# Kernel tuning notes

Hardware: AMD Instinct MI355X
Metric: run time of the kernel (lower is better)

The kernel has to match this reference:

```python
import jax, jax.numpy as jnp
import numpy as np

TOL = 1e-3


def _image_grads(F):
    # replicate-pad central difference, matches GradientBatch (conv with [-0.5,0,0.5])
    Fx = jnp.pad(F, ((0, 0), (0, 0), (0, 0), (1, 1)), mode='edge')
    gx = 0.5 * (Fx[:, :, :, 2:] - Fx[:, :, :, :-2])
    Fy = jnp.pad(F, ((0, 0), (0, 0), (1, 1), (0, 0)), mode='edge')
    gy = 0.5 * (Fy[:, :, 2:, :] - Fy[:, :, :-2, :])
    return gx, gy


def _param_to_H(p):
    B = p.shape[0]
    z = jnp.zeros((B, 1, 1), p.dtype)
    return jnp.concatenate([p, z], 1).reshape(B, 3, 3) + jnp.eye(3, dtype=p.dtype)


def _bilinear_sample(A, xw, yw):
    # grid_sample(mode='bilinear', align_corners=True, padding_mode='zeros') at pixel coords (xw, yw)
    B, k, h, w = A.shape
    x0 = jnp.floor(xw)
    y0 = jnp.floor(yw)
    fx = (xw - x0).reshape(B, 1, h * w)
    fy = (yw - y0).reshape(B, 1, h * w)
    Af = A.reshape(B, k, h * w)

    def gather(xi, yi):
        valid = (xi >= 0) & (xi <= w - 1) & (yi >= 0) & (yi <= h - 1)
        xi_c = jnp.clip(xi, 0, w - 1).astype(jnp.int32)
        yi_c = jnp.clip(yi, 0, h - 1).astype(jnp.int32)
        idx = (yi_c * w + xi_c).reshape(B, 1, h * w)
        v = jnp.take_along_axis(Af, jnp.broadcast_to(idx, (B, k, h * w)), axis=2)
        return v * valid.reshape(B, 1, h * w).astype(A.dtype)

    v00 = gather(x0, y0)
    v01 = gather(x0 + 1, y0)
    v10 = gather(x0, y0 + 1)
    v11 = gather(x0 + 1, y0 + 1)
    Q = ((1 - fx) * (1 - fy) * v00 + fx * (1 - fy) * v01
         + (1 - fx) * fy * v10 + fx * fy * v11)
    return Q.reshape(B, k, h, w)


def _deeplk(img, temp, init_param, max_itr):
    B, k, h, w = temp.shape
    dt = temp.dtype
    gx, gy = _image_grads(temp)
    # centered pixel grid (meshgrid in source: x - x.max()/2)
    x = jnp.arange(w, dtype=dt) - (w - 1) / 2.0
    y = jnp.arange(h, dtype=dt) - (h - 1) / 2.0
    X, Y = jnp.meshgrid(x, y)  # (h, w); X varies along w
    Xf = jnp.tile(X.reshape(-1), k)  # [k*h*w], tiled per channel
    Yf = jnp.tile(Y.reshape(-1), k)
    gxf = gx.reshape(B, k * h * w)
    gyf = gy.reshape(B, k * h * w)
    dIdp = jnp.stack([
        Xf * gxf, Yf * gxf, gxf,
        Xf * gyf, Yf * gyf, gyf,
        -Xf * Xf * gxf - Xf * Yf * gyf,
        -Xf * Yf * gxf - Yf * Yf * gyf,
    ], axis=2)  # [B, k*h*w, 8]
    Hmat = jnp.einsum('bnp,bnq->bpq', dIdp, dIdp)  # [B,8,8]
    invH = jnp.linalg.inv(Hmat)
    invH_dIdp = jnp.einsum('bpq,bnq->bpn', invH, dIdp)  # [B,8,k*h*w]
    xy = jnp.stack([X.reshape(-1), Y.reshape(-1), jnp.ones((h * w,), dt)], 0)  # [3, h*w]
    tolf = jnp.asarray(TOL, dt)

    def step(carry, _):
        p, dp = carry
        Hm = _param_to_H(p)
        xyw = jnp.einsum('bij,jn->bin', Hm, xy)  # [B,3,h*w]
        Xw = (xyw[:, 0] / xyw[:, 2]).reshape(B, h, w) + (w - 1) / 2.0
        Yw = (xyw[:, 1] / xyw[:, 2]).reshape(B, h, w) + (h - 1) / 2.0
        Fi_warp = _bilinear_sample(img, Xw, Yw)
        xn = Xw / ((w - 1) / 2.0) - 1.0
        yn = Yw / ((h - 1) / 2.0) - 1.0
        mask = ((xn > -1 + 2.0 / w) & (xn < 1 - 2.0 / w)
                & (yn > -1 + 2.0 / h) & (yn < 1 - 2.0 / h)).astype(dt)
        r = (Fi_warp - temp * mask[:, None]).reshape(B, k * h * w, 1)
        dp_new = jnp.einsum('bpn,bnj->bpj', invH_dIdp, r)  # [B,8,1]
        dp_new = dp_new.at[:, 6:8, 0].set(0.0)  # zero projective terms
        active = (jnp.linalg.norm(dp, axis=1, keepdims=True) > tolf).astype(dt)
        dp2 = active * dp_new  # converged samples freeze (dp stays 0)
        return (p - dp2, dp2), None

    dp0 = jnp.ones((B, 8, 1), dt)
    (p, _), _ = jax.lax.scan(step, (init_param, dp0), None, length=max_itr)
    return p


def setup_inputs() -> dict:
    key = jax.random.key(0)
    k1, k2 = jax.random.split(key)
    B, k, h, w = 8, 8, 256, 256
    img = jax.random.normal(k1, (B, k, h, w), dtype=jnp.float32)
    temp = jax.random.normal(k2, (B, k, h, w), dtype=jnp.float32)
    init_param = jnp.zeros((B, 8, 1), dtype=jnp.float32)
    return {"img": img, "temp": temp, "init_param": init_param, "max_itr": 10}


def reference(img, temp, init_param, max_itr):
    p = _deeplk(img, temp, init_param, max_itr)
    return (p, _param_to_H(p))
```

## Files before the change

### kernel.cpp

```cpp
#include <hip/hip_runtime.h>
#include <hip/hip_bf16.h>

#define B_ 8
#define K_ 8
#define H_ 256
#define W_ 256
#define HW (H_*W_)

__device__ __forceinline__ unsigned short f2bf(float f) {
    __hip_bfloat16 h = __float2bfloat16(f);
    return *reinterpret_cast<unsigned short*>(&h);
}
__device__ __forceinline__ void ub8(uint4 u, float* o) {
    o[0] = __uint_as_float(u.x << 16); o[1] = __uint_as_float(u.x & 0xffff0000u);
    o[2] = __uint_as_float(u.y << 16); o[3] = __uint_as_float(u.y & 0xffff0000u);
    o[4] = __uint_as_float(u.z << 16); o[5] = __uint_as_float(u.z & 0xffff0000u);
    o[6] = __uint_as_float(u.w << 16); o[7] = __uint_as_float(u.w & 0xffff0000u);
}
__device__ __forceinline__ float half_reduce(float v) {
    v += __shfl_down(v, 16, 64);
    v += __shfl_down(v, 8, 64);
    v += __shfl_down(v, 4, 64);
    v += __shfl_down(v, 2, 64);
    v += __shfl_down(v, 1, 64);
    return v;
}
__device__ __forceinline__ void cstore(float* p, float v) {
    __hip_atomic_store(p, v, __ATOMIC_RELAXED, __HIP_MEMORY_SCOPE_AGENT);
}
__device__ __forceinline__ float cload(const float* p) {
    return __hip_atomic_load((float*)p, __ATOMIC_RELAXED, __HIP_MEMORY_SCOPE_AGENT);
}
__device__ __forceinline__ void wait_count(unsigned int* p, unsigned int target) {
    for (int i = 0; i < 1000000; ++i) {
        if (__hip_atomic_load(p, __ATOMIC_RELAXED, __HIP_MEMORY_SCOPE_AGENT) >= target)
            return;
        __builtin_amdgcn_s_sleep(1);
    }
}

__device__ __forceinline__ void pixel_accum(
    const uint4* __restrict__ imgT,
    const uint4 t0, const uint4 g0, const uint4 g1,
    int b, int x, int y,
    float h00, float h01, float h02, float h10, float h11, float h12,
    float h20, float h21, float* aa) {
    const float X = (float)x - 127.5f, Y = (float)y - 127.5f;
    const float zw = h20 * X + h21 * Y + 1.f;
    const float Xw = (h00 * X + h01 * Y + h02) / zw + 127.5f;
    const float Yw = (h10 * X + h11 * Y + h12) / zw + 127.5f;
    const float NLO = -1.f + 2.f / 256.f, NHI = 1.f - 2.f / 256.f;
    const float xn = Xw / 127.5f - 1.f, yn = Yw / 127.5f - 1.f;
    const float m = (xn > NLO && xn < NHI && yn > NLO && yn < NHI) ? 1.f : 0.f;

    const float x0f = floorf(Xw), y0f = floorf(Yw);
    const float fx = Xw - x0f, fy = Yw - y0f;
    const float x1f = x0f + 1.f, y1f = y0f + 1.f;
    const bool vx0 = (x0f >= 0.f) && (x0f <= 255.f);
    const bool vx1 = (x1f >= 0.f) && (x1f <= 255.f);
    const bool vy0 = (y0f >= 0.f) && (y0f <= 255.f);
    const bool vy1 = (y1f >= 0.f) && (y1f <= 255.f);
    const int xi0 = (int)fminf(fmaxf(x0f, 0.f), 255.f);
    const int xi1 = (int)fminf(fmaxf(x1f, 0.f), 255.f);
    const int yi0 = (int)fminf(fmaxf(y0f, 0.f), 255.f);
    const int yi1 = (int)fminf(fmaxf(y1f, 0.f), 255.f);
    const int i00 = yi0 * W_ + xi0, i01 = yi0 * W_ + xi1;
    const int i10 = yi1 * W_ + xi0, i11 = yi1 * W_ + xi1;
    const float w00 = ((vx0 && vy0) ? 1.f : 0.f) * (1.f - fx) * (1.f - fy);
    const float w01 = ((vx1 && vy0) ? 1.f : 0.f) * fx * (1.f - fy);
    const float w10 = ((vx0 && vy1) ? 1.f : 0.f) * (1.f - fx) * fy;
    const float w11 = ((vx1 && vy1) ? 1.f : 0.f) * fx * fy;

    const int base = b * HW;
    const uint4 u00 = imgT[base + i00], u01 = imgT[base + i01];
    const uint4 u10 = imgT[base + i10], u11 = imgT[base + i11];

    float A00[8], A01[8], A10[8], A11[8], GXa[8], GYa[8], TV[8];
    ub8(u00, A00); ub8(u01, A01); ub8(u10, A10); ub8(u11, A11);
    ub8(t0, TV);   ub8(g0, GXa);  ub8(g1, GYa);

    float vx = 0.f, vy = 0.f;
    #pragma unroll
    for (int c = 0; c < 8; ++c) {
        const float Q = w00 * A00[c] + w01 * A01[c] + w10 * A10[c] + w11 * A11[c];
        const float r = Q - TV[c] * m;
        vx += GXa[c] * r;
        vy += GYa[c] * r;
    }
    const float t0a = X * vx, t4a = Y * vy;
    const float cc = t0a + t4a;
    aa[0] += t0a;      aa[1] += Y * vx;  aa[2] += vx;
    aa[3] += X * vy;   aa[4] += t4a;     aa[5] += vy;
    aa[6] -= X * cc;   aa[7] -= Y * cc;
}

__global__ __launch_bounds__(256) void prep_kernel(
    const float* __restrict__ img, const float* __restrict__ temp,
    uint4* __restrict__ imgT, uint4* __restrict__ TGt,
    uint4* __restrict__ TGx, uint4* __restrict__ TGy,
    double* __restrict__ gramP, unsigned int* __restrict__ bar) {
    __shared__ float smem[8192];
    __shared__ float s15[15];
    const int b   = blockIdx.x & 7;
    const int y   = blockIdx.x >> 3;
    const int tid = threadIdx.x;

    if (blockIdx.x < 8 && tid < 16)
        bar[(blockIdx.x * 16 + tid) * 32] = 0u;

    const int ym = (y > 0) ? y - 1 : 0;
    const int yp = (y < 255) ? y + 1 : 255;

    #pragma unroll
    for (int j = 0; j < 8; ++j) {
        const int slot = tid + 256 * j;
        const int rowid = slot >> 6, col4 = slot & 63;
        const int c = rowid >> 2, sel = rowid & 3;
        const int sy = (sel == 0) ? ym : ((sel == 2) ? yp : y);
        const float* src = ((sel == 3) ? img : temp)
                         + ((size_t)(b * K_ + c) * HW + sy * W_ + col4 * 4);
        const float4 v = *(const float4*)src;
        *(float4*)&smem[(c * 4 + sel) * 256 + col4 * 4] = v;
    }
    __syncthreads();

    const int x = tid;
    const int px = (y << 8) | x;
    const float X = (float)x - 127.5f, Y = (float)y - 127.5f;
    const int xm = (x > 0) ? x - 1 : 0;
    const int xp = (x < 255) ? x + 1 : 255;
    float Sxx = 0.f, Sxy = 0.f, Syy = 0.f;
    unsigned int imgp[4] = {0, 0, 0, 0};
    unsigned int tgp[12];
    #pragma unroll
    for (int i = 0; i < 12; ++i) tgp[i] = 0u;
    #pragma unroll
    for (int c = 0; c < 8; ++c) {
        const float* R = &smem[c * 1024];
        const float gx = 0.5f * (R[256 + xp] - R[256 + xm]);
        const float gy = 0.5f * (R[512 + x] - R[x]);
        const float tc = R[256 + x];
        const float iv = R[768 + x];
        Sxx += gx * gx; Sxy += gx * gy; Syy += gy * gy;
        const int sh = (c & 1) * 16;
        imgp[c >> 1]     |= ((unsigned int)f2bf(iv)) << sh;
        tgp[c >> 1]      |= ((unsigned int)f2bf(tc)) << sh;
        tgp[4 + (c >> 1)]|= ((unsigned int)f2bf(gx)) << sh;
        tgp[8 + (c >> 1)]|= ((unsigned int)f2bf(gy)) << sh;
    }
    const size_t gpx = (size_t)b * HW + px;
    imgT[gpx] = make_uint4(imgp[0], imgp[1], imgp[2], imgp[3]);
    TGt[gpx] = make_uint4(tgp[0], tgp[1], tgp[2],  tgp[3]);
    TGx[gpx] = make_uint4(tgp[4], tgp[5], tgp[6],  tgp[7]);
    TGy[gpx] = make_uint4(tgp[8], tgp[9], tgp[10], tgp[11]);
    __syncthreads();

    {
        const float X2 = X * X;
        const float Xp[5] = {1.f, X, X2, X2 * X, X2 * X2};
        #pragma unroll
        for (int n = 0; n < 5; ++n) {
            smem[n * 256 + tid]        = Sxx * Xp[n];
            smem[(5 + n) * 256 + tid]  = Sxy * Xp[n];
            smem[(10 + n) * 256 + tid] = Syy * Xp[n];
        }
    }
    __syncthreads();
    {
        const int e = tid >> 5, l = tid & 31;
        float v = 0.f;
        #pragma unroll
        for (int j = 0; j < 8; ++j) v += smem[e * 256 + l + 32 * j];
        v = half_reduce(v);
        if ((tid & 31) == 0) s15[e] = v;
    }
    if (tid < 224) {
        const int e = 8 + (tid >> 5), l = tid & 31;
        float v = 0.f;
        #pragma unroll
        for (int j = 0; j < 8; ++j) v += smem[e * 256 + l + 32 * j];
        v = half_reduce(v);
        if ((tid & 31) == 0) s15[e] = v;
    }
    __syncthreads();

    if (tid < 36) {
        const int aC[8]  = {1, 1, 1, 0, 0, 0, -1, -1};
        const int aNX[8] = {1, 0, 0, 0, 0, 0,  2,  1};
        const int aNY[8] = {0, 1, 0, 0, 0, 0,  0,  1};
        const int bC[8]  = {0, 0, 0, 1, 1, 1, -1, -1};
        const int bNX[8] = {0, 0, 0, 1, 0, 0,  1,  0};
        const int bNY[8] = {0, 0, 0, 0, 1, 0,  1,  2};
        const double Yd = (double)Y;
        const double Yp2 = Yd * Yd;
        const double Ypw[5] = {1.0, Yd, Yp2, Yp2 * Yd, Yp2 * Yp2};
        int p = 0, rem = tid;
        while (rem >= 8 - p) { rem -= 8 - p; ++p; }
        const int q = p + rem;
        double g = 0.0;
        const int ac = aC[p] * aC[q];
        if (ac) g += ac * Ypw[aNY[p] + aNY[q]] * (double)s15[aNX[p] + aNX[q]];
        const int ab1 = aC[p] * bC[q];
        if (ab1) g += ab1 * Ypw[aNY[p] + bNY[q]] * (double)s15[5 + aNX[p] + bNX[q]];
        const int ab2 = bC[p] * aC[q];
        if (ab2) g += ab2 * Ypw[bNY[p] + aNY[q]] * (double)s15[5 + bNX[p] + aNX[q]];
        const int bc = bC[p] * bC[q];
        if (bc) g += bc * Ypw[bNY[p] + bNY[q]] * (double)s15[10 + bNX[p] + bNX[q]];
        gramP[((size_t)b * 36 + tid) * 256 + y] = g;
    }
}

__global__ __launch_bounds__(256, 2) void fused_kernel(
    const uint4* __restrict__ imgT,
    const uint4* __restrict__ TGt, const uint4* __restrict__ TGx,
    const uint4* __restrict__ TGy,
    const double* __restrict__ gramP,
    const float* __restrict__ init_param,
    float* __restrict__ sP0, float* __restrict__ sP1,
    unsigned int* __restrict__ bar,
    const int* __restrict__ max_itr, float* __restrict__ out) {
    __shared__ float red[2048];
    __shared__ float s8[8];
    __shared__ double sh_invH[64];
    __shared__ double sh_pd[16];
    __shared__ float sh_pf[8];
    __shared__ double gpart[144];
    __shared__ double shA[64], shB[64];

    const int tid = threadIdx.x;
    const int b   = blockIdx.x & 7;
    const int yb  = blockIdx.x >> 3;
    const int mi_raw = *max_itr;
    const int mi = (mi_raw > 10) ? 10 : mi_raw;

    uint4 rT[4], rGX[4], rGY[4];
    {
        const size_t base = (size_t)b * HW + (size_t)yb * 1024 + tid;
        #pragma unroll
        for (int sub = 0; sub < 4; ++sub) {
            const size_t px = base + (size_t)(sub * 256);
            rT[sub] = TGt[px]; rGX[sub] = TGx[px]; rGY[sub] = TGy[px];
        }
    }

    for (int it = 0; it < mi; ++it) {
        if (it > 0) {
            if (tid == 0) wait_count(&bar[(b * 16 + (it - 1)) * 32], 64u);
            __syncthreads();
            const float* sR = ((it & 1) ? sP0 : sP1) + b * 512;
            const int e = tid >> 5, l = tid & 31;
            float v = cload(&sR[e * 64 + l]) + cload(&sR[e * 64 + 32 + l]);
            v = half_reduce(v);
            if ((tid & 31) == 0) s8[tid >> 5] = v;
            __syncthreads();
            if (tid < 8) {
                double nrm2 = 0.0;
                #pragma unroll
                for (int k2 = 0; k2 < 8; ++k2) {
                    const double d = sh_pd[8 + k2];
                    nrm2 += d * d;
                }
                double dpn = 0.0;
                if (tid < 6) {
                    #pragma unroll
                    for (int k2 = 0; k2 < 8; ++k2)
                        dpn += sh_invH[tid * 8 + k2] * (double)s8[k2];
                }
                const double dp2 = (sqrt(nrm2) > 1e-3) ? dpn : 0.0;
                const double pnew = sh_pd[tid] - dp2;
                sh_pd[tid]     = pnew;
                sh_pd[8 + tid] = dp2;
            }
            __syncthreads();
        } else {
            if (tid < 8) {
                sh_pd[tid]     = (double)init_param[b * 8 + tid];
                sh_pd[8 + tid] = 1.0;
            }
            __syncthreads();
        }

        const float h00 = 1.f + (float)sh_pd[0], h01 = (float)sh_pd[1], h02 = (float)sh_pd[2];
        const float h10 = (float)sh_pd[3], h11 = 1.f + (float)sh_pd[4], h12 = (float)sh_pd[5];
        const float h20 = (float)sh_pd[6], h21 = (float)sh_pd[7];

        float aa[8];
        #pragma unroll
        for (int e = 0; e < 8; ++e) aa[e] = 0.f;
        #pragma unroll
        for (int sub = 0; sub < 4; ++sub) {
            pixel_accum(imgT, rT[sub], rGX[sub], rGY[sub], b, tid, yb * 4 + sub,
                        h00, h01, h02, h10, h11, h12, h20, h21, aa);
        }

        #pragma unroll
        for (int e = 0; e < 8; ++e) red[e * 256 + tid] = aa[e];
        __syncthreads();
        {
            const int e = tid >> 5, l = tid & 31;
            float v = 0.f;
            #pragma unroll
            for (int j = 0; j < 8; ++j) v += red[e * 256 + l + 32 * j];
            v = half_reduce(v);
            if ((tid & 31) == 0) {
                float* sW = (it & 1) ? sP1 : sP0;
                cstore(&sW[b * 512 + e * 64 + yb], v);
            }
        }

        asm volatile("s_waitcnt vmcnt(0)" ::: "memory");
        __syncthreads();
        if (tid == 0)
            __hip_atomic_fetch_add(&bar[(b * 16 + it) * 32], 1u,
                                   __ATOMIC_RELAXED, __HIP_MEMORY_SCOPE_AGENT);

        if (it == 0) {
            if (tid < 144) {
                const int e = tid >> 2, q = tid & 3;
                const double* gp = gramP + ((size_t)b * 36 + e) * 256 + q * 64;
                double acc = 0.0;
                #pragma unroll 8
                for (int i = 0; i < 64; ++i) acc += gp[i];
                gpart[tid] = acc;
            }
            __syncthreads();
            const int i = tid >> 3, j = tid & 7;
            if (tid < 64) {
                const int pp = min(i, j), qq = max(i, j);
                const int tri = 8 * pp - (pp * (pp - 1)) / 2 + (qq - pp);
                shA[tid] = gpart[tri * 4] + gpart[tri * 4 + 1]
                         + gpart[tri * 4 + 2] + gpart[tri * 4 + 3];
                shB[tid] = (i == j) ? 1.0 : 0.0;
            }
            __syncthreads();
            for (int k = 0; k < 8; ++k) {
                const double piv = shA[k * 8 + k];
                __syncthreads();
                if (tid < 64 && i == k) { shA[tid] /= piv; shB[tid] /= piv; }
                __syncthreads();
                double f = 0, ak = 0, bk = 0;
                if (tid < 64) { f = shA[i * 8 + k]; ak = shA[k * 8 + j]; bk = shB[k * 8 + j]; }
                __syncthreads();
                if (tid < 64 && i != k) { shA[tid] -= f * ak; shB[tid] -= f * bk; }
                __syncthreads();
            }
            if (tid < 64) sh_invH[tid] = shB[tid];
            __syncthreads();
        }
    }

    if (yb != 0) return;
    if (mi <= 0) {
        if (tid < 8) out[b * 8 + tid] = init_param[b * 8 + tid];
        if (tid < 9) {
            float v = (tid < 8) ? init_param[b * 8 + tid] : 0.f;
            if (tid == 0 || tid == 4 || tid == 8) v += 1.f;
            out[64 + b * 9 + tid] = v;
        }
        return;
    }
    if (tid == 0) wait_count(&bar[(b * 16 + (mi - 1)) * 32], 64u);
    __syncthreads();
    {
        const float* sb = (((mi - 1) & 1) ? sP1 : sP0) + b * 512;
        const int e = tid >> 5, l = tid & 31;
        float v = cload(&sb[e * 64 + l]) + cload(&sb[e * 64 + 32 + l]);
        v = half_reduce(v);
        if ((tid & 31) == 0) s8[tid >> 5] = v;
    }
    __syncthreads();
    if (tid < 8) {
        double nrm2 = 0.0;
        #pragma unroll
        for (int k2 = 0; k2 < 8; ++k2) {
            const double d = sh_pd[8 + k2];
            nrm2 += d * d;
        }
        double dpn = 0.0;
        if (tid < 6) {
            #pragma unroll
            for (int k2 = 0; k2 < 8; ++k2)
                dpn += sh_invH[tid * 8 + k2] * (double)s8[k2];
        }
        const double dp2 = (sqrt(nrm2) > 1e-3) ? dpn : 0.0;
        const float pf = (float)(sh_pd[tid] - dp2);
        sh_pf[tid] = pf;
        out[b * 8 + tid] = pf;
    }
    __syncthreads();
    if (tid < 9) {
        float v2 = (tid < 8) ? sh_pf[tid] : 0.f;
        if (tid == 0 || tid == 4 || tid == 8) v2 += 1.f;
        out[64 + b * 9 + tid] = v2;
    }
}

extern "C" void kernel_launch(void* const* d_in, const int* in_sizes, int n_in,
                              void* d_out, int out_size, void* d_ws, size_t ws_size,
                              hipStream_t stream) {
    const float* img        = (const float*)d_in[0];
    const float* temp       = (const float*)d_in[1];
    const float* init_param = (const float*)d_in[2];
    const int*   max_itr    = (const int*)d_in[3];
    float* out = (float*)d_out;

    char* w = (char*)d_ws;
    double* gramP = (double*)w;
    float*  sP0   = (float*)(gramP + 73728);
    float*  sP1   = sP0 + 4096;
    unsigned int* bar = (unsigned int*)(sP1 + 4096);
    uint4* imgT   = (uint4*)(w + 1048576);
    uint4* TGt    = (uint4*)(w + 1048576 + 8388608);
    uint4* TGx    = TGt + (size_t)B_ * HW;
    uint4* TGy    = TGx + (size_t)B_ * HW;

    prep_kernel<<<B_ * H_, 256, 0, stream>>>(img, temp, imgT, TGt, TGx, TGy,
                                             gramP, bar);

    void* args[] = {(void*)&imgT, (void*)&TGt, (void*)&TGx, (void*)&TGy,
                    (void*)&gramP, (void*)&init_param, (void*)&sP0, (void*)&sP1,
                    (void*)&bar, (void*)&max_itr, (void*)&out};
    hipError_t err = hipLaunchCooperativeKernel((void*)fused_kernel,
                                                dim3(512), dim3(256),
                                                args, 0, stream);
    if (err != hipSuccess) {
        fused_kernel<<<512, 256, 0, stream>>>(imgT, TGt, TGx, TGy, gramP,
                                              init_param, sP0, sP1, bar,
                                              max_itr, out);
    }
}
```

Before: 186.4 us.

## Fuse prep stage into persistent kernel and keep template gradients in registers

Moves the per-row preprocessing (bf16 packing, gradients, Gram partials) into the persistent iteration kernel, which now runs 512-thread blocks covering four rows each. The packed template and gradient data stay in registers instead of going through global memory, and only the packed image is written out for the gathers. A new grid-wide counter barrier orders the prep stage before the iterations. The Hessian inverse is computed by one block per batch and published through global memory with a flag, so the other blocks no longer each invert it. The change drops the cooperative launch and relies on all 512 blocks being co-resident for the spin barriers, and it adds extra barrier waits.

After: 192.2 us. 3.1% more time.

```diff
diff --git a/kernel.cpp b/kernel.cpp
--- a/kernel.cpp
+++ b/kernel.cpp
@@ -25,11 +25,29 @@
     v += __shfl_down(v, 1, 64);
     return v;
 }
-__device__ __forceinline__ void cstore(float* p, float v) {
+__device__ __forceinline__ float wave_reduce(float v) {
+    v += __shfl_down(v, 32, 64);
+    v += __shfl_down(v, 16, 64);
+    v += __shfl_down(v, 8, 64);
+    v += __shfl_down(v, 4, 64);
+    v += __shfl_down(v, 2, 64);
+    v += __shfl_down(v, 1, 64);
+    return v;
+}
+__device__ __forceinline__ void cstoref(float* p, float v) {
     __hip_atomic_store(p, v, __ATOMIC_RELAXED, __HIP_MEMORY_SCOPE_AGENT);
 }
-__device__ __forceinline__ float cload(const float* p) {
+__device__ __forceinline__ float cloadf(const float* p) {
     return __hip_atomic_load((float*)p, __ATOMIC_RELAXED, __HIP_MEMORY_SCOPE_AGENT);
+}
+__device__ __forceinline__ void cstored(double* p, double v) {
+    __hip_atomic_store(p, v, __ATOMIC_RELAXED, __HIP_MEMORY_SCOPE_AGENT);
+}
+__device__ __forceinline__ double cloadd(const double* p) {
+    return __hip_atomic_load((double*)p, __ATOMIC_RELAXED, __HIP_MEMORY_SCOPE_AGENT);
+}
+__device__ __forceinline__ void cstoreu8(unsigned long long* p, unsigned long long v) {
+    __hip_atomic_store(p, v, __ATOMIC_RELAXED, __HIP_MEMORY_SCOPE_AGENT);
 }
 __device__ __forceinline__ void wait_count(unsigned int* p, unsigned int target) {
     for (int i = 0; i < 1000000; ++i) {
@@ -94,132 +112,19 @@
     aa[6] -= X * cc;   aa[7] -= Y * cc;
 }
 
-__global__ __launch_bounds__(256) void prep_kernel(
+__global__ void zero_bar_kernel(unsigned int* __restrict__ bar) {
+    bar[threadIdx.x * 32] = 0u;
+}
+
+__global__ __launch_bounds__(512, 4) void fused_kernel(
     const float* __restrict__ img, const float* __restrict__ temp,
-    uint4* __restrict__ imgT, uint4* __restrict__ TGt,
-    uint4* __restrict__ TGx, uint4* __restrict__ TGy,
-    double* __restrict__ gramP, unsigned int* __restrict__ bar) {
-    __shared__ float smem[8192];
-    __shared__ float s15[15];
-    const int b   = blockIdx.x & 7;
-    const int y   = blockIdx.x >> 3;
-    const int tid = threadIdx.x;
-
-    if (blockIdx.x < 8 && tid < 16)
-        bar[(blockIdx.x * 16 + tid) * 32] = 0u;
-
-    const int ym = (y > 0) ? y - 1 : 0;
-    const int yp = (y < 255) ? y + 1 : 255;
-
-    #pragma unroll
-    for (int j = 0; j < 8; ++j) {
-        const int slot = tid + 256 * j;
-        const int rowid = slot >> 6, col4 = slot & 63;
-        const int c = rowid >> 2, sel = rowid & 3;
-        const int sy = (sel == 0) ? ym : ((sel == 2) ? yp : y);
-        const float* src = ((sel == 3) ? img : temp)
-                         + ((size_t)(b * K_ + c) * HW + sy * W_ + col4 * 4);
-        const float4 v = *(const float4*)src;
-        *(float4*)&smem[(c * 4 + sel) * 256 + col4 * 4] = v;
-    }
-    __syncthreads();
-
-    const int x = tid;
-    const int px = (y << 8) | x;
-    const float X = (float)x - 127.5f, Y = (float)y - 127.5f;
-    const int xm = (x > 0) ? x - 1 : 0;
-    const int xp = (x < 255) ? x + 1 : 255;
-    float Sxx = 0.f, Sxy = 0.f, Syy = 0.f;
-    unsigned int imgp[4] = {0, 0, 0, 0};
-    unsigned int tgp[12];
-    #pragma unroll
-    for (int i = 0; i < 12; ++i) tgp[i] = 0u;
-    #pragma unroll
-    for (int c = 0; c < 8; ++c) {
-        const float* R = &smem[c * 1024];
-        const float gx = 0.5f * (R[256 + xp] - R[256 + xm]);
-        const float gy = 0.5f * (R[512 + x] - R[x]);
-        const float tc = R[256 + x];
-        const float iv = R[768 + x];
-        Sxx += gx * gx; Sxy += gx * gy; Syy += gy * gy;
-        const int sh = (c & 1) * 16;
-        imgp[c >> 1]     |= ((unsigned int)f2bf(iv)) << sh;
-        tgp[c >> 1]      |= ((unsigned int)f2bf(tc)) << sh;
-        tgp[4 + (c >> 1)]|= ((unsigned int)f2bf(gx)) << sh;
-        tgp[8 + (c >> 1)]|= ((unsigned int)f2bf(gy)) << sh;
-    }
-    const size_t gpx = (size_t)b * HW + px;
-    imgT[gpx] = make_uint4(imgp[0], imgp[1], imgp[2], imgp[3]);
-    TGt[gpx] = make_uint4(tgp[0], tgp[1], tgp[2],  tgp[3]);
-    TGx[gpx] = make_uint4(tgp[4], tgp[5], tgp[6],  tgp[7]);
-    TGy[gpx] = make_uint4(tgp[8], tgp[9], tgp[10], tgp[11]);
-    __syncthreads();
-
-    {
-        const float X2 = X * X;
-        const float Xp[5] = {1.f, X, X2, X2 * X, X2 * X2};
-        #pragma unroll
-        for (int n = 0; n < 5; ++n) {
-            smem[n * 256 + tid]        = Sxx * Xp[n];
-            smem[(5 + n) * 256 + tid]  = Sxy * Xp[n];
-            smem[(10 + n) * 256 + tid] = Syy * Xp[n];
-        }
-    }
-    __syncthreads();
-    {
-        const int e = tid >> 5, l = tid & 31;
-        float v = 0.f;
-        #pragma unroll
-        for (int j = 0; j < 8; ++j) v += smem[e * 256 + l + 32 * j];
-        v = half_reduce(v);
-        if ((tid & 31) == 0) s15[e] = v;
-    }
-    if (tid < 224) {
-        const int e = 8 + (tid >> 5), l = tid & 31;
-        float v = 0.f;
-        #pragma unroll
-        for (int j = 0; j < 8; ++j) v += smem[e * 256 + l + 32 * j];
-        v = half_reduce(v);
-        if ((tid & 31) == 0) s15[e] = v;
-    }
-    __syncthreads();
-
-    if (tid < 36) {
-        const int aC[8]  = {1, 1, 1, 0, 0, 0, -1, -1};
-        const int aNX[8] = {1, 0, 0, 0, 0, 0,  2,  1};
-        const int aNY[8] = {0, 1, 0, 0, 0, 0,  0,  1};
-        const int bC[8]  = {0, 0, 0, 1, 1, 1, -1, -1};
-        const int bNX[8] = {0, 0, 0, 1, 0, 0,  1,  0};
-        const int bNY[8] = {0, 0, 0, 0, 1, 0,  1,  2};
-        const double Yd = (double)Y;
-        const double Yp2 = Yd * Yd;
-        const double Ypw[5] = {1.0, Yd, Yp2, Yp2 * Yd, Yp2 * Yp2};
-        int p = 0, rem = tid;
-        while (rem >= 8 - p) { rem -= 8 - p; ++p; }
-        const int q = p + rem;
-        double g = 0.0;
-        const int ac = aC[p] * aC[q];
-        if (ac) g += ac * Ypw[aNY[p] + aNY[q]] * (double)s15[aNX[p] + aNX[q]];
-        const int ab1 = aC[p] * bC[q];
-        if (ab1) g += ab1 * Ypw[aNY[p] + bNY[q]] * (double)s15[5 + aNX[p] + bNX[q]];
-        const int ab2 = bC[p] * aC[q];
-        if (ab2) g += ab2 * Ypw[bNY[p] + aNY[q]] * (double)s15[5 + bNX[p] + aNX[q]];
-        const int bc = bC[p] * bC[q];
-        if (bc) g += bc * Ypw[bNY[p] + bNY[q]] * (double)s15[10 + bNX[p] + bNX[q]];
-        gramP[((size_t)b * 36 + tid) * 256 + y] = g;
-    }
-}
-
-__global__ __launch_bounds__(256, 2) void fused_kernel(
-    const uint4* __restrict__ imgT,
-    const uint4* __restrict__ TGt, const uint4* __restrict__ TGx,
-    const uint4* __restrict__ TGy,
-    const double* __restrict__ gramP,
-    const float* __restrict__ init_param,
+    uint4* __restrict__ imgT, double* __restrict__ gramP,
+    double* __restrict__ invHg, const float* __restrict__ init_param,
     float* __restrict__ sP0, float* __restrict__ sP1,
     unsigned int* __restrict__ bar,
     const int* __restrict__ max_itr, float* __restrict__ out) {
-    __shared__ float red[2048];
+    __shared__ float smem[16384];
+    __shared__ float s15s[2][15];
     __shared__ float s8[8];
     __shared__ double sh_invH[64];
     __shared__ double sh_pd[16];
@@ -230,28 +135,147 @@
     const int tid = threadIdx.x;
     const int b   = blockIdx.x & 7;
     const int yb  = blockIdx.x >> 3;
+    const int h   = tid >> 8;
+    const int t2  = tid & 255;
     const int mi_raw = *max_itr;
     const int mi = (mi_raw > 10) ? 10 : mi_raw;
 
-    uint4 rT[4], rGX[4], rGY[4];
-    {
-        const size_t base = (size_t)b * HW + (size_t)yb * 1024 + tid;
-        #pragma unroll
-        for (int sub = 0; sub < 4; ++sub) {
-            const size_t px = base + (size_t)(sub * 256);
-            rT[sub] = TGt[px]; rGX[sub] = TGx[px]; rGY[sub] = TGy[px];
-        }
-    }
+    uint4 rT[2], rGX[2], rGY[2];
+    float* region = &smem[h * 8192];
+    #pragma unroll
+    for (int rl = 0; rl < 2; ++rl) {
+        const int row = h + 2 * rl;
+        const int y   = yb * 4 + row;
+        const int ym = (y > 0) ? y - 1 : 0;
+        const int yp = (y < 255) ? y + 1 : 255;
+        __syncthreads();
+        #pragma unroll
+        for (int j = 0; j < 8; ++j) {
+            const int slot = t2 + 256 * j;
+            const int rowid = slot >> 6, col4 = slot & 63;
+            const int c = rowid >> 2, sel = rowid & 3;
+            const int sy = (sel == 0) ? ym : ((sel == 2) ? yp : y);
+            const float* src = ((sel == 3) ? img : temp)
+                             + ((size_t)(b * K_ + c) * HW + sy * W_ + col4 * 4);
+            const float4 v = *(const float4*)src;
+            *(float4*)&region[(c * 4 + sel) * 256 + col4 * 4] = v;
+        }
+        __syncthreads();
+
+        const int x = t2;
+        const int xm = (x > 0) ? x - 1 : 0;
+        const int xp = (x < 255) ? x + 1 : 255;
+        float Sxx = 0.f, Sxy = 0.f, Syy = 0.f;
+        unsigned int imgp[4] = {0, 0, 0, 0};
+        unsigned int tgp[12];
+        #pragma unroll
+        for (int i = 0; i < 12; ++i) tgp[i] = 0u;
+        #pragma unroll
+        for (int c = 0; c < 8; ++c) {
+            const float* R = &region[c * 1024];
+            const float gx = 0.5f * (R[256 + xp] - R[256 + xm]);
+            const float gy = 0.5f * (R[512 + x] - R[x]);
+            const float tc = R[256 + x];
+            const float iv = R[768 + x];
+            Sxx += gx * gx; Sxy += gx * gy; Syy += gy * gy;
+            const int sh = (c & 1) * 16;
+            imgp[c >> 1]     |= ((unsigned int)f2bf(iv)) << sh;
+            tgp[c >> 1]      |= ((unsigned int)f2bf(tc)) << sh;
+            tgp[4 + (c >> 1)]|= ((unsigned int)f2bf(gx)) << sh;
+            tgp[8 + (c >> 1)]|= ((unsigned int)f2bf(gy)) << sh;
+        }
+        {
+            const size_t gpx = (size_t)b * HW + (size_t)y * W_ + x;
+            unsigned long long* ip = (unsigned long long*)(imgT + gpx);
+            cstoreu8(ip,     ((unsigned long long)imgp[1] << 32) | imgp[0]);
+            cstoreu8(ip + 1, ((unsigned long long)imgp[3] << 32) | imgp[2]);
+        }
+        rT[rl]  = make_uint4(tgp[0], tgp[1], tgp[2],  tgp[3]);
+        rGX[rl] = make_uint4(tgp[4], tgp[5], tgp[6],  tgp[7]);
+        rGY[rl] = make_uint4(tgp[8], tgp[9], tgp[10], tgp[11]);
+        __syncthreads();
+
+        {
+            const float X = (float)x - 127.5f;
+            const float X2 = X * X;
+            const float Xp[5] = {1.f, X, X2, X2 * X, X2 * X2};
+            #pragma unroll
+            for (int n = 0; n < 5; ++n) {
+                region[n * 256 + t2]        = Sxx * Xp[n];
+                region[(5 + n) * 256 + t2]  = Sxy * Xp[n];
+                region[(10 + n) * 256 + t2] = Syy * Xp[n];
+            }
+        }
+        __syncthreads();
+        {
+            const int e = t2 >> 5, l = t2 & 31;
+            float v = 0.f;
+            #pragma unroll
+            for (int j = 0; j < 8; ++j) v += region[e * 256 + l + 32 * j];
+            v = half_reduce(v);
+            if (l == 0) s15s[h][e] = v;
+        }
+        if (t2 < 224) {
+            const int e = 8 + (t2 >> 5), l = t2 & 31;
+            float v = 0.f;
+            #pragma unroll
+            for (int j = 0; j < 8; ++j) v += region[e * 256 + l + 32 * j];
+            v = half_reduce(v);
+            if (l == 0) s15s[h][e] = v;
+        }
+        __syncthreads();
+
+        if (t2 < 36) {
+            const int aC[8]  = {1, 1, 1, 0, 0, 0, -1, -1};
+            const int aNX[8] = {1, 0, 0, 0, 0, 0,  2,  1};
+            const int aNY[8] = {0, 1, 0, 0, 0, 0,  0,  1};
+            const int bC[8]  = {0, 0, 0, 1, 1, 1, -1, -1};
+            const int bNX[8] = {0, 0, 0, 1, 0, 0,  1,  0};
+            const int bNY[8] = {0, 0, 0, 0, 1, 0,  1,  2};
+            const float* s15 = s15s[h];
+            const double Yd = (double)((float)y - 127.5f);
+            const double Yp2 = Yd * Yd;
+            const double Ypw[5] = {1.0, Yd, Yp2, Yp2 * Yd, Yp2 * Yp2};
+            int p = 0, rem = t2;
+            while (rem >= 8 - p) { rem -= 8 - p; ++p; }
+            const int q = p + rem;
+            double g = 0.0;
+            const int ac = aC[p] * aC[q];
+            if (ac) g += ac * Ypw[aNY[p] + aNY[q]] * (double)s15[aNX[p] + aNX[q]];
+            const int ab1 = aC[p] * bC[q];
+            if (ab1) g += ab1 * Ypw[aNY[p] + bNY[q]] * (double)s15[5 + aNX[p] + bNX[q]];
+            const int ab2 = bC[p] * aC[q];
+            if (ab2) g += ab2 * Ypw[bNY[p] + aNY[q]] * (double)s15[5 + bNX[p] + aNX[q]];
+            const int bc = bC[p] * bC[q];
+            if (bc) g += bc * Ypw[bNY[p] + bNY[q]] * (double)s15[10 + bNX[p] + bNX[q]];
+            cstored(&gramP[((size_t)b * 36 + t2) * 256 + y], g);
+        }
+    }
+
+    asm volatile("s_waitcnt vmcnt(0)" ::: "memory");
+    __syncthreads();
+    if (tid == 0) {
+        __hip_atomic_fetch_add(&bar[(b * 16 + 10) * 32], 1u,
+                               __ATOMIC_RELAXED, __HIP_MEMORY_SCOPE_AGENT);
+        wait_count(&bar[(b * 16 + 10) * 32], 64u);
+    }
+    __syncthreads();
 
     for (int it = 0; it < mi; ++it) {
         if (it > 0) {
-            if (tid == 0) wait_count(&bar[(b * 16 + (it - 1)) * 32], 64u);
-            __syncthreads();
-            const float* sR = ((it & 1) ? sP0 : sP1) + b * 512;
-            const int e = tid >> 5, l = tid & 31;
-            float v = cload(&sR[e * 64 + l]) + cload(&sR[e * 64 + 32 + l]);
-            v = half_reduce(v);
-            if ((tid & 31) == 0) s8[tid >> 5] = v;
+            if (tid == 0) {
+                wait_count(&bar[(b * 16 + (it - 1)) * 32], 64u);
+                if (it == 1) wait_count(&bar[(b * 16 + 11) * 32], 1u);
+            }
+            __syncthreads();
+            if (it == 1 && tid < 64) sh_invH[tid] = cloadd(&invHg[b * 64 + tid]);
+            {
+                const float* sR = ((it & 1) ? sP0 : sP1) + b * 512;
+                const int e = tid >> 6, l = tid & 63;
+                float v = cloadf(&sR[e * 64 + l]);
+                v = wave_reduce(v);
+                if (l == 0) s8[e] = v;
+            }
             __syncthreads();
             if (tid < 8) {
                 double nrm2 = 0.0;
@@ -288,23 +312,26 @@
         #pragma unroll
         for (int e = 0; e < 8; ++e) aa[e] = 0.f;
         #pragma unroll
-        for (int sub = 0; sub < 4; ++sub) {
-            pixel_accum(imgT, rT[sub], rGX[sub], rGY[sub], b, tid, yb * 4 + sub,
+        for (int sub = 0; sub < 2; ++sub) {
+            const int pxl = tid + 512 * sub;
+            pixel_accum(imgT, rT[sub], rGX[sub], rGY[sub], b,
+                        pxl & 255, yb * 4 + (pxl >> 8),
                         h00, h01, h02, h10, h11, h12, h20, h21, aa);
         }
 
-        #pragma unroll
-        for (int e = 0; e < 8; ++e) red[e * 256 + tid] = aa[e];
+        float* red = smem;
+        #pragma unroll
+        for (int e = 0; e < 8; ++e) red[e * 512 + tid] = aa[e];
         __syncthreads();
         {
-            const int e = tid >> 5, l = tid & 31;
+            const int e = tid >> 6, l = tid & 63;
             float v = 0.f;
             #pragma unroll
-            for (int j = 0; j < 8; ++j) v += red[e * 256 + l + 32 * j];
-            v = half_reduce(v);
-            if ((tid & 31) == 0) {
+            for (int j = 0; j < 8; ++j) v += red[e * 512 + l + 64 * j];
+            v = wave_reduce(v);
+            if (l == 0) {
                 float* sW = (it & 1) ? sP1 : sP0;
-                cstore(&sW[b * 512 + e * 64 + yb], v);
+                cstoref(&sW[b * 512 + e * 64 + yb], v);
             }
         }
 
@@ -314,13 +341,13 @@
             __hip_atomic_fetch_add(&bar[(b * 16 + it) * 32], 1u,
                                    __ATOMIC_RELAXED, __HIP_MEMORY_SCOPE_AGENT);
 
-        if (it == 0) {
+        if (it == 0 && yb == 0) {
             if (tid < 144) {
                 const int e = tid >> 2, q = tid & 3;
                 const double* gp = gramP + ((size_t)b * 36 + e) * 256 + q * 64;
                 double acc = 0.0;
                 #pragma unroll 8
-                for (int i = 0; i < 64; ++i) acc += gp[i];
+                for (int i = 0; i < 64; ++i) acc += cloadd(&gp[i]);
                 gpart[tid] = acc;
             }
             __syncthreads();
@@ -344,8 +371,12 @@
                 if (tid < 64 && i != k) { shA[tid] -= f * ak; shB[tid] -= f * bk; }
                 __syncthreads();
             }
-            if (tid < 64) sh_invH[tid] = shB[tid];
-            __syncthreads();
+            if (tid < 64) cstored(&invHg[b * 64 + tid], shB[tid]);
+            asm volatile("s_waitcnt vmcnt(0)" ::: "memory");
+            __syncthreads();
+            if (tid == 0)
+                __hip_atomic_fetch_add(&bar[(b * 16 + 11) * 32], 1u,
+                                       __ATOMIC_RELAXED, __HIP_MEMORY_SCOPE_AGENT);
         }
     }
 
@@ -361,12 +392,15 @@
     }
     if (tid == 0) wait_count(&bar[(b * 16 + (mi - 1)) * 32], 64u);
     __syncthreads();
+    if (mi == 1) {
+        if (tid < 64) sh_invH[tid] = cloadd(&invHg[b * 64 + tid]);
+    }
     {
         const float* sb = (((mi - 1) & 1) ? sP1 : sP0) + b * 512;
-        const int e = tid >> 5, l = tid & 31;
-        float v = cload(&sb[e * 64 + l]) + cload(&sb[e * 64 + 32 + l]);
-        v = half_reduce(v);
-        if ((tid & 31) == 0) s8[tid >> 5] = v;
+        const int e = tid >> 6, l = tid & 63;
+        float v = cloadf(&sb[e * 64 + l]);
+        v = wave_reduce(v);
+        if (l == 0) s8[e] = v;
     }
     __syncthreads();
     if (tid < 8) {
@@ -406,26 +440,14 @@
 
     char* w = (char*)d_ws;
     double* gramP = (double*)w;
-    float*  sP0   = (float*)(gramP + 73728);
+    double* invHg = gramP + 73728;
+    float*  sP0   = (float*)(invHg + 512);
     float*  sP1   = sP0 + 4096;
     unsigned int* bar = (unsigned int*)(sP1 + 4096);
     uint4* imgT   = (uint4*)(w + 1048576);
-    uint4* TGt    = (uint4*)(w + 1048576 + 8388608);
-    uint4* TGx    = TGt + (size_t)B_ * HW;
-    uint4* TGy    = TGx + (size_t)B_ * HW;
-
-    prep_kernel<<<B_ * H_, 256, 0, stream>>>(img, temp, imgT, TGt, TGx, TGy,
-                                             gramP, bar);
-
-    void* args[] = {(void*)&imgT, (void*)&TGt, (void*)&TGx, (void*)&TGy,
-                    (void*)&gramP, (void*)&init_param, (void*)&sP0, (void*)&sP1,
-                    (void*)&bar, (void*)&max_itr, (void*)&out};
-    hipError_t err = hipLaunchCooperativeKernel((void*)fused_kernel,
-                                                dim3(512), dim3(256),
-                                                args, 0, stream);
-    if (err != hipSuccess) {
-        fused_kernel<<<512, 256, 0, stream>>>(imgT, TGt, TGx, TGy, gramP,
-                                              init_param, sP0, sP1, bar,
-                                              max_itr, out);
-    }
-}
+
+    zero_bar_kernel<<<1, 128, 0, stream>>>(bar);
+    fused_kernel<<<512, 512, 0, stream>>>(img, temp, imgT, gramP, invHg,
+                                          init_param, sP0, sP1, bar,
+                                          max_itr, out);
+}
```

## Replace atomic barrier counter with per-block flags and compute invH once per batch

Applied to the files above, without the earlier changes.

Swaps the per-iteration atomic fetch_add counter for per-block flag words that 64 lanes poll together with a ballot, which removes atomic contention on a single address. The 8x8 Gauss-Jordan inverse of H now runs only in the yb==0 block of each batch and is published to the other blocks through global memory plus a flag, where before every block inverted it redundantly. The cooperative launch is replaced by a plain launch and the spin timeout is shortened, so correctness now depends on all 512 blocks being co-resident. The bf16 unpacking is also rewritten as per-channel extraction.

Measured after the change: 156.8 us (median of 2 runs). 1.19x faster.

```diff
diff --git a/kernel.cpp b/kernel.cpp
--- a/kernel.cpp
+++ b/kernel.cpp
@@ -11,11 +11,9 @@
     __hip_bfloat16 h = __float2bfloat16(f);
     return *reinterpret_cast<unsigned short*>(&h);
 }
-__device__ __forceinline__ void ub8(uint4 u, float* o) {
-    o[0] = __uint_as_float(u.x << 16); o[1] = __uint_as_float(u.x & 0xffff0000u);
-    o[2] = __uint_as_float(u.y << 16); o[3] = __uint_as_float(u.y & 0xffff0000u);
-    o[4] = __uint_as_float(u.z << 16); o[5] = __uint_as_float(u.z & 0xffff0000u);
-    o[6] = __uint_as_float(u.w << 16); o[7] = __uint_as_float(u.w & 0xffff0000u);
+__device__ __forceinline__ float bfex(uint4 u, int c) {
+    const unsigned int w = (&u.x)[c >> 1];
+    return __uint_as_float((c & 1) ? (w & 0xffff0000u) : (w << 16));
 }
 __device__ __forceinline__ float half_reduce(float v) {
     v += __shfl_down(v, 16, 64);
@@ -25,16 +23,34 @@
     v += __shfl_down(v, 1, 64);
     return v;
 }
-__device__ __forceinline__ void cstore(float* p, float v) {
+__device__ __forceinline__ void cstoref(float* p, float v) {
     __hip_atomic_store(p, v, __ATOMIC_RELAXED, __HIP_MEMORY_SCOPE_AGENT);
 }
-__device__ __forceinline__ float cload(const float* p) {
+__device__ __forceinline__ float cloadf(const float* p) {
     return __hip_atomic_load((float*)p, __ATOMIC_RELAXED, __HIP_MEMORY_SCOPE_AGENT);
 }
+__device__ __forceinline__ void cstored(double* p, double v) {
+    __hip_atomic_store(p, v, __ATOMIC_RELAXED, __HIP_MEMORY_SCOPE_AGENT);
+}
+__device__ __forceinline__ double cloadd(const double* p) {
+    return __hip_atomic_load((double*)p, __ATOMIC_RELAXED, __HIP_MEMORY_SCOPE_AGENT);
+}
+__device__ __forceinline__ void cstoreu(unsigned int* p, unsigned int v) {
+    __hip_atomic_store(p, v, __ATOMIC_RELAXED, __HIP_MEMORY_SCOPE_AGENT);
+}
+__device__ __forceinline__ unsigned int cloadu(const unsigned int* p) {
+    return __hip_atomic_load((unsigned int*)p, __ATOMIC_RELAXED, __HIP_MEMORY_SCOPE_AGENT);
+}
 __device__ __forceinline__ void wait_count(unsigned int* p, unsigned int target) {
-    for (int i = 0; i < 1000000; ++i) {
-        if (__hip_atomic_load(p, __ATOMIC_RELAXED, __HIP_MEMORY_SCOPE_AGENT) >= target)
-            return;
+    for (int i = 0; i < 20000; ++i) {
+        if (cloadu(p) >= target) return;
+        __builtin_amdgcn_s_sleep(1);
+    }
+}
+__device__ __forceinline__ void wait_flags64(unsigned int* base, int lane) {
+    for (int i = 0; i < 20000; ++i) {
+        const unsigned int v = cloadu(base + lane * 16);
+        if (!__ballot(v == 0u)) return;
         __builtin_amdgcn_s_sleep(1);
     }
 }
@@ -75,17 +91,14 @@
     const uint4 u00 = imgT[base + i00], u01 = imgT[base + i01];
     const uint4 u10 = imgT[base + i10], u11 = imgT[base + i11];
 
-    float A00[8], A01[8], A10[8], A11[8], GXa[8], GYa[8], TV[8];
-    ub8(u00, A00); ub8(u01, A01); ub8(u10, A10); ub8(u11, A11);
-    ub8(t0, TV);   ub8(g0, GXa);  ub8(g1, GYa);
-
     float vx = 0.f, vy = 0.f;
     #pragma unroll
     for (int c = 0; c < 8; ++c) {
-        const float Q = w00 * A00[c] + w01 * A01[c] + w10 * A10[c] + w11 * A11[c];
-        const float r = Q - TV[c] * m;
-        vx += GXa[c] * r;
-        vy += GYa[c] * r;
+        const float Q = w00 * bfex(u00, c) + w01 * bfex(u01, c)
+                      + w10 * bfex(u10, c) + w11 * bfex(u11, c);
+        const float r = Q - bfex(t0, c) * m;
+        vx += bfex(g0, c) * r;
+        vy += bfex(g1, c) * r;
     }
     const float t0a = X * vx, t4a = Y * vy;
     const float cc = t0a + t4a;
@@ -98,15 +111,20 @@
     const float* __restrict__ img, const float* __restrict__ temp,
     uint4* __restrict__ imgT, uint4* __restrict__ TGt,
     uint4* __restrict__ TGx, uint4* __restrict__ TGy,
-    double* __restrict__ gramP, unsigned int* __restrict__ bar) {
+    double* __restrict__ gramP,
+    unsigned int* __restrict__ iterFlags, unsigned int* __restrict__ invHflag) {
     __shared__ float smem[8192];
     __shared__ float s15[15];
     const int b   = blockIdx.x & 7;
     const int y   = blockIdx.x >> 3;
     const int tid = threadIdx.x;
 
-    if (blockIdx.x < 8 && tid < 16)
-        bar[(blockIdx.x * 16 + tid) * 32] = 0u;
+    if (blockIdx.x < 8) {
+        for (int s = tid; s < 641; s += 256) {
+            if (s < 640) iterFlags[((size_t)blockIdx.x * 640 + s) * 16] = 0u;
+            else         invHflag[blockIdx.x * 16] = 0u;
+        }
+    }
 
     const int ym = (y > 0) ? y - 1 : 0;
     const int yp = (y < 255) ? y + 1 : 255;
@@ -172,7 +190,7 @@
         #pragma unroll
         for (int j = 0; j < 8; ++j) v += smem[e * 256 + l + 32 * j];
         v = half_reduce(v);
-        if ((tid & 31) == 0) s15[e] = v;
+        if (l == 0) s15[e] = v;
     }
     if (tid < 224) {
         const int e = 8 + (tid >> 5), l = tid & 31;
@@ -214,10 +232,10 @@
     const uint4* __restrict__ imgT,
     const uint4* __restrict__ TGt, const uint4* __restrict__ TGx,
     const uint4* __restrict__ TGy,
-    const double* __restrict__ gramP,
+    const double* __restrict__ gramP, double* __restrict__ invHg,
     const float* __restrict__ init_param,
     float* __restrict__ sP0, float* __restrict__ sP1,
-    unsigned int* __restrict__ bar,
+    unsigned int* __restrict__ iterFlags, unsigned int* __restrict__ invHflag,
     const int* __restrict__ max_itr, float* __restrict__ out) {
     __shared__ float red[2048];
     __shared__ float s8[8];
@@ -245,13 +263,17 @@
 
     for (int it = 0; it < mi; ++it) {
         if (it > 0) {
-            if (tid == 0) wait_count(&bar[(b * 16 + (it - 1)) * 32], 64u);
-            __syncthreads();
-            const float* sR = ((it & 1) ? sP0 : sP1) + b * 512;
-            const int e = tid >> 5, l = tid & 31;
-            float v = cload(&sR[e * 64 + l]) + cload(&sR[e * 64 + 32 + l]);
-            v = half_reduce(v);
-            if ((tid & 31) == 0) s8[tid >> 5] = v;
+            if (tid < 64) wait_flags64(&iterFlags[(size_t)(b * 640 + (it - 1) * 64) * 16], tid);
+            if (it == 1 && tid == 0) wait_count(&invHflag[b * 16], 1u);
+            __syncthreads();
+            if (it == 1 && tid < 64) sh_invH[tid] = cloadd(&invHg[b * 64 + tid]);
+            {
+                const float* sR = ((it & 1) ? sP0 : sP1) + b * 512;
+                const int e = tid >> 5, l = tid & 31;
+                float v = cloadf(&sR[e * 64 + l]) + cloadf(&sR[e * 64 + 32 + l]);
+                v = half_reduce(v);
+                if (l == 0) s8[e] = v;
+            }
             __syncthreads();
             if (tid < 8) {
                 double nrm2 = 0.0;
@@ -302,19 +324,18 @@
             #pragma unroll
             for (int j = 0; j < 8; ++j) v += red[e * 256 + l + 32 * j];
             v = half_reduce(v);
-            if ((tid & 31) == 0) {
+            if (l == 0) {
                 float* sW = (it & 1) ? sP1 : sP0;
-                cstore(&sW[b * 512 + e * 64 + yb], v);
+                cstoref(&sW[b * 512 + e * 64 + yb], v);
             }
         }
 
         asm volatile("s_waitcnt vmcnt(0)" ::: "memory");
         __syncthreads();
         if (tid == 0)
-            __hip_atomic_fetch_add(&bar[(b * 16 + it) * 32], 1u,
-                                   __ATOMIC_RELAXED, __HIP_MEMORY_SCOPE_AGENT);
-
-        if (it == 0) {
+            cstoreu(&iterFlags[(size_t)(b * 640 + it * 64 + yb) * 16], 1u);
+
+        if (it == 0 && yb == 0) {
             if (tid < 144) {
                 const int e = tid >> 2, q = tid & 3;
                 const double* gp = gramP + ((size_t)b * 36 + e) * 256 + q * 64;
@@ -344,8 +365,11 @@
                 if (tid < 64 && i != k) { shA[tid] -= f * ak; shB[tid] -= f * bk; }
                 __syncthreads();
             }
-            if (tid < 64) sh_invH[tid] = shB[tid];
-            __syncthreads();
+            if (tid < 64) { cstored(&invHg[b * 64 + tid], shB[tid]);
+                            sh_invH[tid] = shB[tid]; }
+            asm volatile("s_waitcnt vmcnt(0)" ::: "memory");
+            __syncthreads();
+            if (tid == 0) cstoreu(&invHflag[b * 16], 1u);
         }
     }
 
@@ -359,14 +383,14 @@
         }
         return;
     }
-    if (tid == 0) wait_count(&bar[(b * 16 + (mi - 1)) * 32], 64u);
+    if (tid < 64) wait_flags64(&iterFlags[(size_t)(b * 640 + (mi - 1) * 64) * 16], tid);
     __syncthreads();
     {
         const float* sb = (((mi - 1) & 1) ? sP1 : sP0) + b * 512;
         const int e = tid >> 5, l = tid & 31;
-        float v = cload(&sb[e * 64 + l]) + cload(&sb[e * 64 + 32 + l]);
+        float v = cloadf(&sb[e * 64 + l]) + cloadf(&sb[e * 64 + 32 + l]);
         v = half_reduce(v);
-        if ((tid & 31) == 0) s8[tid >> 5] = v;
+        if (l == 0) s8[e] = v;
     }
     __syncthreads();
     if (tid < 8) {
@@ -406,26 +430,19 @@
 
     char* w = (char*)d_ws;
     double* gramP = (double*)w;
-    float*  sP0   = (float*)(gramP + 73728);
+    double* invHg = gramP + 73728;
+    float*  sP0   = (float*)(invHg + 512);
     float*  sP1   = sP0 + 4096;
-    unsigned int* bar = (unsigned int*)(sP1 + 4096);
+    unsigned int* iterFlags = (unsigned int*)(sP1 + 4096);
+    unsigned int* invHflag  = iterFlags + 8 * 640 * 16;
     uint4* imgT   = (uint4*)(w + 1048576);
     uint4* TGt    = (uint4*)(w + 1048576 + 8388608);
     uint4* TGx    = TGt + (size_t)B_ * HW;
     uint4* TGy    = TGx + (size_t)B_ * HW;
 
     prep_kernel<<<B_ * H_, 256, 0, stream>>>(img, temp, imgT, TGt, TGx, TGy,
-                                             gramP, bar);
-
-    void* args[] = {(void*)&imgT, (void*)&TGt, (void*)&TGx, (void*)&TGy,
-                    (void*)&gramP, (void*)&init_param, (void*)&sP0, (void*)&sP1,
-                    (void*)&bar, (void*)&max_itr, (void*)&out};
-    hipError_t err = hipLaunchCooperativeKernel((void*)fused_kernel,
-                                                dim3(512), dim3(256),
-                                                args, 0, stream);
-    if (err != hipSuccess) {
-        fused_kernel<<<512, 256, 0, stream>>>(imgT, TGt, TGx, TGy, gramP,
-                                              init_param, sP0, sP1, bar,
-                                              max_itr, out);
-    }
-}
+                                             gramP, iterFlags, invHflag);
+    fused_kernel<<<512, 256, 0, stream>>>(imgT, TGt, TGx, TGy, gramP, invHg,
+                                          init_param, sP0, sP1,
+                                          iterFlags, invHflag, max_itr, out);
+}
```
